# Optimization experiments

Hardware: AMD Instinct MI355X
Metric: run time of the kernel (lower is better)

## Reference

```python
import jax, jax.numpy as jnp
import numpy as np

B, N, M, K = 2, 16384, 16384, 32
C_IN, C_OUT, KS = 64, 128, 15
RADIUS = 0.1
SIGMA = 0.5 * RADIUS  # module sets self.sigma = sigma * radius


def _generate_kernel_points(num_kpoints: int, radius: float) -> np.ndarray:
    # Fibonacci-sphere placement, matching the torch generate_kernel_points
    if num_kpoints == 1:
        return np.zeros((1, 3), dtype=np.float32)
    pts = np.zeros((num_kpoints, 3), dtype=np.float32)
    golden_angle = np.pi * (3 - np.sqrt(5))
    for i in range(num_kpoints):
        y = 1 - i / float(num_kpoints - 1) * 2
        r_y = np.sqrt(1 - y * y)
        theta = golden_angle * i
        pts[i] = np.array([np.cos(theta) * r_y, y, np.sin(theta) * r_y]) * radius
    return pts


def setup_inputs() -> dict:
    key = jax.random.key(0)
    k1, k2, k3, k4 = jax.random.split(key, 4)
    query_points = jax.random.uniform(k1, (B, N, 3), dtype=jnp.float32)
    support_points = jax.random.uniform(k2, (B, M, 3), dtype=jnp.float32)
    support_features = jax.random.normal(k3, (B, M, C_IN), dtype=jnp.float32)
    neighbor_idx = jax.random.randint(k4, (B, N, K), 0, M)
    kernel_points = jnp.asarray(_generate_kernel_points(KS, RADIUS * 0.8))
    k5 = jax.random.fold_in(key, 5)
    # kaiming-uniform-ish init on flattened (KS*C_IN, C_OUT)
    bound = np.sqrt(1.0 / (KS * C_IN))
    weights = jax.random.uniform(k5, (KS, C_IN, C_OUT), dtype=jnp.float32,
                                 minval=-bound, maxval=bound)
    bias = jnp.zeros((C_OUT,), dtype=jnp.float32)
    return {
        "query_points": query_points,
        "support_points": support_points,
        "support_features": support_features,
        "neighbor_idx": neighbor_idx,
        "kernel_points": kernel_points,
        "weights": weights,
        "bias": bias,
    }


def reference(query_points, support_points, support_features, neighbor_idx,
              kernel_points, weights, bias):
    # Batched gather: support[b, idx[b]] -> [B, N, K, *]
    gather = jax.vmap(lambda feats, idx: feats[idx])
    neighbor_points = gather(support_points, neighbor_idx)      # [B,N,K,3]
    neighbor_features = gather(support_features, neighbor_idx)  # [B,N,K,C_in]

    rel = neighbor_points - query_points[:, :, None, :]          # [B,N,K,3]
    # squared distance to each kernel point: [B,N,K,J]
    sq_dist = jnp.sum((rel[:, :, :, None, :] - kernel_points[None, None, None]) ** 2,
                      axis=-1)
    influences = jnp.exp(-sq_dist / (2 * SIGMA ** 2))
    influences = influences / (influences.sum(axis=-1, keepdims=True) + 1e-6)

    out = jnp.einsum('bnkc,bnkj,jco->bno', neighbor_features, influences, weights)
    return out + bias
```

## Files before the change

### kernel.cpp

```cpp
#include <hip/hip_runtime.h>
#include <hip/hip_bf16.h>


#define NB   16384
#define MB   16384
#define KN   32
#define CIN  64
#define COUT 128
#define KS   15
#define TP   16
#define WF_BYTES  245760u
#define FP_BYTES  (2u * MB * CIN * 2u)
#define SP4_BYTES (2u * MB * 16u)

typedef __attribute__((ext_vector_type(8))) short short8;
typedef __attribute__((ext_vector_type(4))) float f32x4;

#define ROR_ADD(s, ctrl) \
    ((s) + __int_as_float(__builtin_amdgcn_update_dpp( \
        0, __float_as_int(s), (ctrl), 0xF, 0xF, true)))

static __device__ __forceinline__ unsigned int pack2_bf16(float f0, float f1) {
    const unsigned int a = __float_as_uint(f0) + 0x8000u;
    const unsigned int b = __float_as_uint(f1) + 0x8000u;
    return (a >> 16) | (b & 0xffff0000u);
}

static __device__ __forceinline__ unsigned int pack2_bf16_rne(float f0, float f1) {
    unsigned int a = __float_as_uint(f0);
    unsigned int b = __float_as_uint(f1);
    a += 0x7fffu + ((a >> 16) & 1u);
    b += 0x7fffu + ((b >> 16) & 1u);
    return (a >> 16) | (b & 0xffff0000u);
}

static __device__ __forceinline__ unsigned short f32_to_bf16_rne(float x) {
    unsigned int u = __float_as_uint(x);
    u += 0x7fffu + ((u >> 16) & 1u);
    return (unsigned short)(u >> 16);
}

__global__ __launch_bounds__(256)
void prep_kernel(const float* __restrict__ Wg, const float* __restrict__ feats,
                 const float* __restrict__ sp,
                 unsigned short* __restrict__ wf, unsigned int* __restrict__ fp,
                 float4* __restrict__ sp4, int full) {
    const int bid = blockIdx.x;
    if (bid < 60) {
        const int tid = bid * 256 + threadIdx.x;
        const int l = tid & 63;
        const int t = (tid >> 6) & 7;
        const int s = tid >> 9;
        const int n  = t * 16 + (l & 15);
        const int kb = s * 32 + (l >> 4) * 8;
        short8 o;
        #pragma unroll
        for (int i = 0; i < 8; ++i)
            o[i] = (short)f32_to_bf16_rne(Wg[(kb + i) * COUT + n]);
        *(short8*)(wf + (size_t)tid * 8) = o;
    } else if (!full) {
        return;
    } else if (bid < 60 + 128) {
        const int m = (bid - 60) * 256 + threadIdx.x;
        const float* s3 = sp + 3 * (size_t)m;
        sp4[m] = make_float4(s3[0], s3[1], s3[2], 0.0f);
    } else {
        const unsigned int t = (unsigned int)(bid - 188) * 256u + threadIdx.x;
        if (t < 2u * MB * 32u) {
            const int m   = t >> 5;
            const int p2  = t & 31;
            const int n16 = p2 >> 1;
            const int tt  = (p2 & 1) * 2;
            const float a = feats[(size_t)m * CIN + tt * 16 + n16];
            const float b = feats[(size_t)m * CIN + (tt + 1) * 16 + n16];
            fp[t] = pack2_bf16_rne(a, b);
        }
    }
}

template<bool PK>
__global__ __launch_bounds__(512, 6)
void kpconv_mfma(const float* __restrict__ qp,
                 const float* __restrict__ sp,
                 const float* __restrict__ feats,
                 const unsigned int* __restrict__ fpk,
                 const float4* __restrict__ sp4,
                 const int* __restrict__ nidx,
                 const float* __restrict__ kp,
                 const unsigned short* __restrict__ wfrag,
                 const float* __restrict__ bias,
                 float* __restrict__ out) {
    __shared__ __align__(16) char sF[16 * 2048];

    const int tid  = threadIdx.x;
    const int lane = tid & 63;
    const int wv   = tid >> 6;
    const int gp_base = blockIdx.x * TP;
    const int b = gp_base >> 14;
    const float*        fbf  = feats + (size_t)b * MB * CIN;
    const unsigned int* fpb  = fpk + (size_t)b * MB * 32;
    const float4*       sp4b = sp4 + (size_t)b * MB;
    const float*        spb  = sp + (size_t)b * MB * 3;

    const int n16  = lane & 15;
    const int quad = lane >> 4;

    float kxj, kyj, kzj;
    if (n16 < 15) {
        kxj = kp[3 * n16 + 0];
        kyj = kp[3 * n16 + 1];
        kzj = kp[3 * n16 + 2];
    } else {
        kxj = 1.0e4f; kyj = 1.0e4f; kzj = 1.0e4f;
    }

    const int gp0 = gp_base + wv * 2;
    const int* ip = nidx + (size_t)gp0 * KN + quad * 8;

    int idx0[8], idx1[8];
    *(int4*)(&idx0[0]) = *(const int4*)(ip);
    *(int4*)(&idx0[4]) = *(const int4*)(ip + 4);
    *(int4*)(&idx1[0]) = *(const int4*)(ip + KN);
    *(int4*)(&idx1[4]) = *(const int4*)(ip + KN + 4);

    #pragma unroll
    for (int pt = 0; pt < 2; ++pt) {
        const int pl = wv * 2 + pt;
        const int gp = gp0 + pt;
        const int* idxv = pt ? idx1 : idx0;

        const float qx = qp[3 * gp + 0];
        const float qy = qp[3 * gp + 1];
        const float qz = qp[3 * gp + 2];
        const float qkx = qx + kxj, qky = qy + kyj, qkz = qz + kzj;

        float e[8];
        uint2 g[8];
        if (PK) {
            float4 s4[8];
            #pragma unroll
            for (int i = 0; i < 8; ++i) s4[i] = sp4b[idxv[i]];
            #pragma unroll
            for (int i = 0; i < 8; ++i)
                g[i] = *(const uint2*)(fpb + (size_t)idxv[i] * 32 + n16 * 2);
            #pragma unroll
            for (int i = 0; i < 8; ++i) {
                const float dx = s4[i].x - qkx;
                const float dy = s4[i].y - qky;
                const float dz = s4[i].z - qkz;
                const float d2 = fmaf(dx, dx, fmaf(dy, dy, dz * dz));
                e[i] = __expf(-200.0f * d2);
            }
        } else {
            #pragma unroll
            for (int i = 0; i < 8; ++i) {
                const float* s3 = spb + (size_t)idxv[i] * 3;
                const float dx = s3[0] - qkx;
                const float dy = s3[1] - qky;
                const float dz = s3[2] - qkz;
                const float d2 = fmaf(dx, dx, fmaf(dy, dy, dz * dz));
                e[i] = __expf(-200.0f * d2);
            }
        }

        unsigned int iu[4];
        float en[8];
        #pragma unroll
        for (int i = 0; i < 8; ++i) {
            float s = e[i];
            s = ROR_ADD(s, 0x128);
            s = ROR_ADD(s, 0x124);
            s = ROR_ADD(s, 0x122);
            s = ROR_ADD(s, 0x121);
            en[i] = e[i] * __builtin_amdgcn_rcpf(s + 1e-6f);
        }
        #pragma unroll
        for (int ih = 0; ih < 4; ++ih)
            iu[ih] = pack2_bf16(en[2 * ih], en[2 * ih + 1]);
        const short8 ifrag = *(const short8*)iu;

        unsigned int fu[4][4];
        if (PK) {
            #pragma unroll
            for (int ih = 0; ih < 4; ++ih) {
                const unsigned int ax = g[2 * ih].x, bx = g[2 * ih + 1].x;
                const unsigned int ay = g[2 * ih].y, by = g[2 * ih + 1].y;
                fu[0][ih] = __builtin_amdgcn_perm(bx, ax, 0x05040100u);
                fu[1][ih] = __builtin_amdgcn_perm(bx, ax, 0x07060302u);
                fu[2][ih] = __builtin_amdgcn_perm(by, ay, 0x05040100u);
                fu[3][ih] = __builtin_amdgcn_perm(by, ay, 0x07060302u);
            }
        } else {
            #pragma unroll
            for (int ih = 0; ih < 4; ++ih) {
                const float* fr0 = fbf + (size_t)idxv[2 * ih]     * CIN + n16;
                const float* fr1 = fbf + (size_t)idxv[2 * ih + 1] * CIN + n16;
                #pragma unroll
                for (int t = 0; t < 4; ++t)
                    fu[t][ih] = pack2_bf16(fr0[t * 16], fr1[t * 16]);
            }
        }

        #pragma unroll
        for (int t = 0; t < 4; ++t) {
            const short8 ffrag = *(const short8*)(fu[t]);
            f32x4 z = {0.f, 0.f, 0.f, 0.f};
            const f32x4 dd = __builtin_amdgcn_mfma_f32_16x16x32_bf16(ffrag, ifrag, z, 0, 0, 0);
            const unsigned int lo = pack2_bf16(dd[0], dd[1]);
            const unsigned int hi = pack2_bf16(dd[2], dd[3]);
            const int off = n16 * 2048 + (t * 2 + (quad >> 1)) * 256 +
                            ((pl ^ (n16 & 7)) * 16) + (quad & 1) * 8;
            uint2 v; v.x = lo; v.y = hi;
            *(uint2*)(sF + off) = v;
        }
    }
    __syncthreads();

    f32x4 acc = {0.f, 0.f, 0.f, 0.f};

    #pragma unroll
    for (int s = 0; s < 30; ++s) {
        const int j = s >> 1;
        const int u = (s & 1) * 4 + quad;
        const int off = j * 2048 + u * 256 + ((n16 ^ (j & 7)) * 16);
        const short8 a  = *(const short8*)(sF + off);
        const short8 bf = *(const short8*)(wfrag + ((size_t)(s * 8 + wv) * 64 + lane) * 8);
        acc = __builtin_amdgcn_mfma_f32_16x16x32_bf16(a, bf, acc, 0, 0, 0);
    }

    const float bsv = bias[wv * 16 + n16];
    #pragma unroll
    for (int r = 0; r < 4; ++r) {
        out[(size_t)(gp_base + quad * 4 + r) * COUT + wv * 16 + n16] = acc[r] + bsv;
    }
}

extern "C" void kernel_launch(void* const* d_in, const int* in_sizes, int n_in,
                              void* d_out, int out_size, void* d_ws, size_t ws_size,
                              hipStream_t stream) {
    const float* qp = (const float*)d_in[0];
    const float* sp = (const float*)d_in[1];
    const float* ft = (const float*)d_in[2];
    const int*   ni = (const int*)d_in[3];
    const float* kp = (const float*)d_in[4];
    const float* wg = (const float*)d_in[5];
    const float* bs = (const float*)d_in[6];
    float* o = (float*)d_out;

    unsigned short* wfrag = (unsigned short*)d_ws;
    unsigned int*   fpk   = (unsigned int*)((char*)d_ws + WF_BYTES);
    float4*         sp4   = (float4*)((char*)d_ws + WF_BYTES + FP_BYTES);
    const int full = (ws_size >= (size_t)(WF_BYTES + FP_BYTES + SP4_BYTES)) ? 1 : 0;

    const int prep_blocks = full ? (60 + 128 + 4096) : 60;
    hipLaunchKernelGGL(prep_kernel, dim3(prep_blocks), dim3(256), 0, stream,
                       wg, ft, sp, wfrag, fpk, sp4, full);

    if (full) {
        hipLaunchKernelGGL((kpconv_mfma<true>), dim3((2 * NB) / TP), dim3(512), 0, stream,
                           qp, sp, ft, fpk, sp4, ni, kp, wfrag, bs, o);
    } else {
        hipLaunchKernelGGL((kpconv_mfma<false>), dim3((2 * NB) / TP), dim3(512), 0, stream,
                           qp, sp, ft, fpk, sp4, ni, kp, wfrag, bs, o);
    }
}
```

Baseline: 115.7 us.

## Process 32 points per block and software-pipeline neighbor gathers

Doubles the number of query points per block from 16 to 32, so each wave handles four points and the second-stage GEMM reuses each weight fragment load for two MFMAs. This halves weight-fragment traffic per point. It also software-pipelines the gather, prefetching the next point's neighbor indices and support-point coordinates while the current point is computed. In exchange it doubles LDS use, lowers the launch-bounds occupancy target from 6 to 4, and raises register pressure.

```diff
diff --git a/kernel.cpp b/kernel.cpp
--- a/kernel.cpp
+++ b/kernel.cpp
@@ -8,7 +8,7 @@
 #define CIN  64
 #define COUT 128
 #define KS   15
-#define TP   16
+#define TP   32
 #define WF_BYTES  245760u
 #define FP_BYTES  (2u * MB * CIN * 2u)
 #define SP4_BYTES (2u * MB * 16u)
@@ -79,7 +79,7 @@
 }
 
 template<bool PK>
-__global__ __launch_bounds__(512, 6)
+__global__ __launch_bounds__(512, 4)
 void kpconv_mfma(const float* __restrict__ qp,
                  const float* __restrict__ sp,
                  const float* __restrict__ feats,
@@ -90,7 +90,7 @@
                  const unsigned short* __restrict__ wfrag,
                  const float* __restrict__ bias,
                  float* __restrict__ out) {
-    __shared__ __align__(16) char sF[16 * 2048];
+    __shared__ __align__(16) char sF[16 * 4096];
 
     const int tid  = threadIdx.x;
     const int lane = tid & 63;
@@ -114,20 +114,44 @@
         kxj = 1.0e4f; kyj = 1.0e4f; kzj = 1.0e4f;
     }
 
-    const int gp0 = gp_base + wv * 2;
+    const int gp0 = gp_base + wv * 4;
     const int* ip = nidx + (size_t)gp0 * KN + quad * 8;
 
-    int idx0[8], idx1[8];
-    *(int4*)(&idx0[0]) = *(const int4*)(ip);
-    *(int4*)(&idx0[4]) = *(const int4*)(ip + 4);
-    *(int4*)(&idx1[0]) = *(const int4*)(ip + KN);
-    *(int4*)(&idx1[4]) = *(const int4*)(ip + KN + 4);
+    int idxc[8], idxn[8];
+    *(int4*)(&idxc[0]) = *(const int4*)(ip);
+    *(int4*)(&idxc[4]) = *(const int4*)(ip + 4);
+
+    float4 s4c[8];
+    if (PK) {
+        #pragma unroll
+        for (int i = 0; i < 8; ++i) s4c[i] = sp4b[idxc[i]];
+    }
+    *(int4*)(&idxn[0]) = *(const int4*)(ip + KN);
+    *(int4*)(&idxn[4]) = *(const int4*)(ip + KN + 4);
 
     #pragma unroll
-    for (int pt = 0; pt < 2; ++pt) {
-        const int pl = wv * 2 + pt;
+    for (int pt = 0; pt < 4; ++pt) {
+        const int pl = wv * 4 + pt;
         const int gp = gp0 + pt;
-        const int* idxv = pt ? idx1 : idx0;
+
+        uint2 g[8];
+        if (PK) {
+            #pragma unroll
+            for (int i = 0; i < 8; ++i)
+                g[i] = *(const uint2*)(fpb + (size_t)idxc[i] * 32 + n16 * 2);
+        }
+
+        float4 s4n[8];
+        if (PK && pt < 3) {
+            #pragma unroll
+            for (int i = 0; i < 8; ++i) s4n[i] = sp4b[idxn[i]];
+        }
+        int idx2[8];
+        if (pt < 2) {
+            const int* ip2 = ip + (pt + 2) * KN;
+            *(int4*)(&idx2[0]) = *(const int4*)(ip2);
+            *(int4*)(&idx2[4]) = *(const int4*)(ip2 + 4);
+        }
 
         const float qx = qp[3 * gp + 0];
         const float qy = qp[3 * gp + 1];
@@ -135,26 +159,19 @@
         const float qkx = qx + kxj, qky = qy + kyj, qkz = qz + kzj;
 
         float e[8];
-        uint2 g[8];
         if (PK) {
-            float4 s4[8];
-            #pragma unroll
-            for (int i = 0; i < 8; ++i) s4[i] = sp4b[idxv[i]];
-            #pragma unroll
-            for (int i = 0; i < 8; ++i)
-                g[i] = *(const uint2*)(fpb + (size_t)idxv[i] * 32 + n16 * 2);
             #pragma unroll
             for (int i = 0; i < 8; ++i) {
-                const float dx = s4[i].x - qkx;
-                const float dy = s4[i].y - qky;
-                const float dz = s4[i].z - qkz;
+                const float dx = s4c[i].x - qkx;
+                const float dy = s4c[i].y - qky;
+                const float dz = s4c[i].z - qkz;
                 const float d2 = fmaf(dx, dx, fmaf(dy, dy, dz * dz));
                 e[i] = __expf(-200.0f * d2);
             }
         } else {
             #pragma unroll
             for (int i = 0; i < 8; ++i) {
-                const float* s3 = spb + (size_t)idxv[i] * 3;
+                const float* s3 = spb + (size_t)idxc[i] * 3;
                 const float dx = s3[0] - qkx;
                 const float dy = s3[1] - qky;
                 const float dz = s3[2] - qkz;
@@ -193,8 +210,8 @@
         } else {
             #pragma unroll
             for (int ih = 0; ih < 4; ++ih) {
-                const float* fr0 = fbf + (size_t)idxv[2 * ih]     * CIN + n16;
-                const float* fr1 = fbf + (size_t)idxv[2 * ih + 1] * CIN + n16;
+                const float* fr0 = fbf + (size_t)idxc[2 * ih]     * CIN + n16;
+                const float* fr1 = fbf + (size_t)idxc[2 * ih + 1] * CIN + n16;
                 #pragma unroll
                 for (int t = 0; t < 4; ++t)
                     fu[t][ih] = pack2_bf16(fr0[t * 16], fr1[t * 16]);
@@ -208,30 +225,47 @@
             const f32x4 dd = __builtin_amdgcn_mfma_f32_16x16x32_bf16(ffrag, ifrag, z, 0, 0, 0);
             const unsigned int lo = pack2_bf16(dd[0], dd[1]);
             const unsigned int hi = pack2_bf16(dd[2], dd[3]);
-            const int off = n16 * 2048 + (t * 2 + (quad >> 1)) * 256 +
+            const int off = n16 * 4096 + (t * 2 + (quad >> 1)) * 512 +
                             ((pl ^ (n16 & 7)) * 16) + (quad & 1) * 8;
             uint2 v; v.x = lo; v.y = hi;
             *(uint2*)(sF + off) = v;
         }
+
+        if (pt < 3) {
+            #pragma unroll
+            for (int i = 0; i < 8; ++i) {
+                if (PK) s4c[i] = s4n[i];
+                idxc[i] = idxn[i];
+            }
+            if (pt < 2) {
+                #pragma unroll
+                for (int i = 0; i < 8; ++i) idxn[i] = idx2[i];
+            }
+        }
     }
     __syncthreads();
 
-    f32x4 acc = {0.f, 0.f, 0.f, 0.f};
+    f32x4 acc0 = {0.f, 0.f, 0.f, 0.f};
+    f32x4 acc1 = {0.f, 0.f, 0.f, 0.f};
 
     #pragma unroll
     for (int s = 0; s < 30; ++s) {
         const int j = s >> 1;
         const int u = (s & 1) * 4 + quad;
-        const int off = j * 2048 + u * 256 + ((n16 ^ (j & 7)) * 16);
-        const short8 a  = *(const short8*)(sF + off);
+        const int off0 = j * 4096 + u * 512 + ((n16 ^ (j & 7)) * 16);
+        const short8 a0 = *(const short8*)(sF + off0);
+        const short8 a1 = *(const short8*)(sF + off0 + 256);
         const short8 bf = *(const short8*)(wfrag + ((size_t)(s * 8 + wv) * 64 + lane) * 8);
-        acc = __builtin_amdgcn_mfma_f32_16x16x32_bf16(a, bf, acc, 0, 0, 0);
+        acc0 = __builtin_amdgcn_mfma_f32_16x16x32_bf16(a0, bf, acc0, 0, 0, 0);
+        acc1 = __builtin_amdgcn_mfma_f32_16x16x32_bf16(a1, bf, acc1, 0, 0, 0);
     }
 
     const float bsv = bias[wv * 16 + n16];
     #pragma unroll
     for (int r = 0; r < 4; ++r) {
-        out[(size_t)(gp_base + quad * 4 + r) * COUT + wv * 16 + n16] = acc[r] + bsv;
+        const int pr = quad * 4 + r;
+        out[(size_t)(gp_base + pr)      * COUT + wv * 16 + n16] = acc0[r] + bsv;
+        out[(size_t)(gp_base + 16 + pr) * COUT + wv * 16 + n16] = acc1[r] + bsv;
     }
 }
 
```

New measurement: 109.2 us. 5.7% less time.

## Process two 16-point halves per block with double-buffered LDS software pipeline

Applied to the files above, without the earlier changes.

Each block now handles 32 query points in two halves, each with its own LDS buffer. The index and support-point gathers for the second half are issued before the first half's weight MFMA stage, so global gather latency overlaps with matrix work. The cost is double the LDS footprint (64KB), a lower occupancy hint, and half as many blocks. The launch configuration must also change to match the new block size.

```diff
diff --git a/kernel.cpp b/kernel.cpp
--- a/kernel.cpp
+++ b/kernel.cpp
@@ -8,7 +8,7 @@
 #define CIN  64
 #define COUT 128
 #define KS   15
-#define TP   16
+#define TP   32
 #define WF_BYTES  245760u
 #define FP_BYTES  (2u * MB * CIN * 2u)
 #define SP4_BYTES (2u * MB * 16u)
@@ -79,7 +79,7 @@
 }
 
 template<bool PK>
-__global__ __launch_bounds__(512, 6)
+__global__ __launch_bounds__(512, 4)
 void kpconv_mfma(const float* __restrict__ qp,
                  const float* __restrict__ sp,
                  const float* __restrict__ feats,
@@ -90,7 +90,7 @@
                  const unsigned short* __restrict__ wfrag,
                  const float* __restrict__ bias,
                  float* __restrict__ out) {
-    __shared__ __align__(16) char sF[16 * 2048];
+    __shared__ __align__(16) char sF[2 * 32768];
 
     const int tid  = threadIdx.x;
     const int lane = tid & 63;
@@ -113,21 +113,40 @@
     } else {
         kxj = 1.0e4f; kyj = 1.0e4f; kzj = 1.0e4f;
     }
-
-    const int gp0 = gp_base + wv * 2;
-    const int* ip = nidx + (size_t)gp0 * KN + quad * 8;
-
-    int idx0[8], idx1[8];
-    *(int4*)(&idx0[0]) = *(const int4*)(ip);
-    *(int4*)(&idx0[4]) = *(const int4*)(ip + 4);
-    *(int4*)(&idx1[0]) = *(const int4*)(ip + KN);
-    *(int4*)(&idx1[4]) = *(const int4*)(ip + KN + 4);
-
-    #pragma unroll
-    for (int pt = 0; pt < 2; ++pt) {
-        const int pl = wv * 2 + pt;
-        const int gp = gp0 + pt;
-        const int* idxv = pt ? idx1 : idx0;
+    const float bsv = bias[wv * 16 + n16];
+
+    int idxA[8], idxB[8];
+    float4 s4A[8];
+
+    auto loadPair = [&](int h) {
+        const int gp = gp_base + h * 16 + wv * 2;
+        const int* ipp = nidx + (size_t)gp * KN + quad * 8;
+        *(int4*)(&idxA[0]) = *(const int4*)(ipp);
+        *(int4*)(&idxA[4]) = *(const int4*)(ipp + 4);
+        *(int4*)(&idxB[0]) = *(const int4*)(ipp + KN);
+        *(int4*)(&idxB[4]) = *(const int4*)(ipp + KN + 4);
+    };
+
+    auto gatherSp4 = [&](const int* idxv, float4* s4) {
+        if (PK) {
+            #pragma unroll
+            for (int i = 0; i < 8; ++i) s4[i] = sp4b[idxv[i]];
+        } else {
+            #pragma unroll
+            for (int i = 0; i < 8; ++i) {
+                const float* s3 = spb + (size_t)idxv[i] * 3;
+                s4[i] = make_float4(s3[0], s3[1], s3[2], 0.0f);
+            }
+        }
+    };
+
+    auto aPoint = [&](const int* idxv, const float4* s4, int h, int plh, int gp) {
+        uint2 g[8];
+        if (PK) {
+            #pragma unroll
+            for (int i = 0; i < 8; ++i)
+                g[i] = *(const uint2*)(fpb + (size_t)idxv[i] * 32 + n16 * 2);
+        }
 
         const float qx = qp[3 * gp + 0];
         const float qy = qp[3 * gp + 1];
@@ -135,32 +154,13 @@
         const float qkx = qx + kxj, qky = qy + kyj, qkz = qz + kzj;
 
         float e[8];
-        uint2 g[8];
-        if (PK) {
-            float4 s4[8];
-            #pragma unroll
-            for (int i = 0; i < 8; ++i) s4[i] = sp4b[idxv[i]];
-            #pragma unroll
-            for (int i = 0; i < 8; ++i)
-                g[i] = *(const uint2*)(fpb + (size_t)idxv[i] * 32 + n16 * 2);
-            #pragma unroll
-            for (int i = 0; i < 8; ++i) {
-                const float dx = s4[i].x - qkx;
-                const float dy = s4[i].y - qky;
-                const float dz = s4[i].z - qkz;
-                const float d2 = fmaf(dx, dx, fmaf(dy, dy, dz * dz));
-                e[i] = __expf(-200.0f * d2);
-            }
-        } else {
-            #pragma unroll
-            for (int i = 0; i < 8; ++i) {
-                const float* s3 = spb + (size_t)idxv[i] * 3;
-                const float dx = s3[0] - qkx;
-                const float dy = s3[1] - qky;
-                const float dz = s3[2] - qkz;
-                const float d2 = fmaf(dx, dx, fmaf(dy, dy, dz * dz));
-                e[i] = __expf(-200.0f * d2);
-            }
+        #pragma unroll
+        for (int i = 0; i < 8; ++i) {
+            const float dx = s4[i].x - qkx;
+            const float dy = s4[i].y - qky;
+            const float dz = s4[i].z - qkz;
+            const float d2 = fmaf(dx, dx, fmaf(dy, dy, dz * dz));
+            e[i] = __expf(-200.0f * d2);
         }
 
         unsigned int iu[4];
@@ -201,6 +201,7 @@
             }
         }
 
+        char* base = sF + h * 32768;
         #pragma unroll
         for (int t = 0; t < 4; ++t) {
             const short8 ffrag = *(const short8*)(fu[t]);
@@ -209,30 +210,50 @@
             const unsigned int lo = pack2_bf16(dd[0], dd[1]);
             const unsigned int hi = pack2_bf16(dd[2], dd[3]);
             const int off = n16 * 2048 + (t * 2 + (quad >> 1)) * 256 +
-                            ((pl ^ (n16 & 7)) * 16) + (quad & 1) * 8;
+                            ((plh ^ (n16 & 7)) * 16) + (quad & 1) * 8;
             uint2 v; v.x = lo; v.y = hi;
-            *(uint2*)(sF + off) = v;
-        }
-    }
+            *(uint2*)(base + off) = v;
+        }
+    };
+
+    auto aHalf = [&](int h) {
+        float4 s4B[8];
+        gatherSp4(idxB, s4B);
+        aPoint(idxA, s4A, h, wv * 2,     gp_base + h * 16 + wv * 2);
+        aPoint(idxB, s4B, h, wv * 2 + 1, gp_base + h * 16 + wv * 2 + 1);
+    };
+
+    auto bHalf = [&](int h) {
+        f32x4 acc = {0.f, 0.f, 0.f, 0.f};
+        const char* base = sF + h * 32768;
+        #pragma unroll
+        for (int s = 0; s < 30; ++s) {
+            const int j = s >> 1;
+            const int u = (s & 1) * 4 + quad;
+            const short8 a  = *(const short8*)(base + j * 2048 + u * 256 +
+                                               ((n16 ^ (j & 7)) * 16));
+            const short8 bf = *(const short8*)(wfrag +
+                                ((size_t)(s * 8 + wv) * 64 + lane) * 8);
+            acc = __builtin_amdgcn_mfma_f32_16x16x32_bf16(a, bf, acc, 0, 0, 0);
+        }
+        #pragma unroll
+        for (int r = 0; r < 4; ++r)
+            out[(size_t)(gp_base + h * 16 + quad * 4 + r) * COUT + wv * 16 + n16]
+                = acc[r] + bsv;
+    };
+
+    loadPair(0);
+    gatherSp4(idxA, s4A);
+    aHalf(0);
     __syncthreads();
 
-    f32x4 acc = {0.f, 0.f, 0.f, 0.f};
-
-    #pragma unroll
-    for (int s = 0; s < 30; ++s) {
-        const int j = s >> 1;
-        const int u = (s & 1) * 4 + quad;
-        const int off = j * 2048 + u * 256 + ((n16 ^ (j & 7)) * 16);
-        const short8 a  = *(const short8*)(sF + off);
-        const short8 bf = *(const short8*)(wfrag + ((size_t)(s * 8 + wv) * 64 + lane) * 8);
-        acc = __builtin_amdgcn_mfma_f32_16x16x32_bf16(a, bf, acc, 0, 0, 0);
-    }
-
-    const float bsv = bias[wv * 16 + n16];
-    #pragma unroll
-    for (int r = 0; r < 4; ++r) {
-        out[(size_t)(gp_base + quad * 4 + r) * COUT + wv * 16 + n16] = acc[r] + bsv;
-    }
+    loadPair(1);
+    gatherSp4(idxA, s4A);
+    bHalf(0);
+    aHalf(1);
+    __syncthreads();
+
+    bHalf(1);
 }
 
 extern "C" void kernel_launch(void* const* d_in, const int* in_sizes, int n_in,
```

Result: slower. 131.6 us (+13.7%).

## Process two point tiles per block with double-buffered LDS to overlap gathers

Applied to the files above, without the earlier changes.

Each block now handles 32 query points in two halves of 16, using two LDS buffers. The index loads and support-point gathers for the second half are issued before the first half's weight GEMM, so gather latency can overlap MFMA work. Occupancy drops from 6 to 4 blocks per CU in launch bounds and LDS use doubles. The interpolation code is also restructured to interleave pairs of DPP reductions for more instruction-level parallelism.

```diff
diff --git a/kernel.cpp b/kernel.cpp
--- a/kernel.cpp
+++ b/kernel.cpp
@@ -8,7 +8,7 @@
 #define CIN  64
 #define COUT 128
 #define KS   15
-#define TP   16
+#define TP   32
 #define WF_BYTES  245760u
 #define FP_BYTES  (2u * MB * CIN * 2u)
 #define SP4_BYTES (2u * MB * 16u)
@@ -78,8 +78,121 @@
     }
 }
 
+
+#define LOAD_IDX_PAIR(IDX0, IDX1, GPH)                                        \
+    {                                                                         \
+        const int* ipp_ = nidx + (size_t)(GPH) * KN + quad * 8;               \
+        *(int4*)(&IDX0[0]) = *(const int4*)(ipp_);                            \
+        *(int4*)(&IDX0[4]) = *(const int4*)(ipp_ + 4);                        \
+        *(int4*)(&IDX1[0]) = *(const int4*)(ipp_ + KN);                       \
+        *(int4*)(&IDX1[4]) = *(const int4*)(ipp_ + KN + 4);                   \
+    }
+
+#define GATHER_SP4(IDXV, S4V)                                                 \
+    {                                                                         \
+        if (PK) {                                                             \
+            _Pragma("unroll")                                                 \
+            for (int i_ = 0; i_ < 8; ++i_) S4V[i_] = sp4b[IDXV[i_]];          \
+        } else {                                                              \
+            _Pragma("unroll")                                                 \
+            for (int i_ = 0; i_ < 8; ++i_) {                                  \
+                const float* s3_ = spb + (size_t)IDXV[i_] * 3;                \
+                S4V[i_] = make_float4(s3_[0], s3_[1], s3_[2], 0.0f);          \
+            }                                                                 \
+        }                                                                     \
+    }
+
+#define A_POINT(IDXV, S4V, BASE, PLH, GP)                                     \
+    {                                                                         \
+        uint2 g_[8];                                                          \
+        if (PK) {                                                             \
+            _Pragma("unroll")                                                 \
+            for (int i_ = 0; i_ < 8; ++i_)                                    \
+                g_[i_] = *(const uint2*)(fpb + (size_t)IDXV[i_] * 32 + n16 * 2); \
+        }                                                                     \
+        const float qx_ = qp[3 * (GP) + 0];                                   \
+        const float qy_ = qp[3 * (GP) + 1];                                   \
+        const float qz_ = qp[3 * (GP) + 2];                                   \
+        const float qkx_ = qx_ + kxj, qky_ = qy_ + kyj, qkz_ = qz_ + kzj;     \
+        float e_[8];                                                          \
+        _Pragma("unroll")                                                     \
+        for (int i_ = 0; i_ < 8; ++i_) {                                      \
+            const float dx_ = S4V[i_].x - qkx_;                               \
+            const float dy_ = S4V[i_].y - qky_;                               \
+            const float dz_ = S4V[i_].z - qkz_;                               \
+            const float d2_ = fmaf(dx_, dx_, fmaf(dy_, dy_, dz_ * dz_));      \
+            e_[i_] = __expf(-200.0f * d2_);                                   \
+        }                                                                     \
+        unsigned int iu_[4];                                                  \
+        _Pragma("unroll")                                                     \
+        for (int ih_ = 0; ih_ < 4; ++ih_) {                                   \
+            float s0_ = e_[2 * ih_], s1_ = e_[2 * ih_ + 1];                   \
+            s0_ = ROR_ADD(s0_, 0x128); s1_ = ROR_ADD(s1_, 0x128);             \
+            s0_ = ROR_ADD(s0_, 0x124); s1_ = ROR_ADD(s1_, 0x124);             \
+            s0_ = ROR_ADD(s0_, 0x122); s1_ = ROR_ADD(s1_, 0x122);             \
+            s0_ = ROR_ADD(s0_, 0x121); s1_ = ROR_ADD(s1_, 0x121);             \
+            const float n0_ = e_[2 * ih_]     * __builtin_amdgcn_rcpf(s0_ + 1e-6f); \
+            const float n1_ = e_[2 * ih_ + 1] * __builtin_amdgcn_rcpf(s1_ + 1e-6f); \
+            iu_[ih_] = pack2_bf16(n0_, n1_);                                  \
+        }                                                                     \
+        const short8 ifrag_ = *(const short8*)iu_;                            \
+        unsigned int fu_[4][4];                                               \
+        if (PK) {                                                             \
+            _Pragma("unroll")                                                 \
+            for (int ih_ = 0; ih_ < 4; ++ih_) {                               \
+                const unsigned int ax_ = g_[2 * ih_].x, bx_ = g_[2 * ih_ + 1].x; \
+                const unsigned int ay_ = g_[2 * ih_].y, by_ = g_[2 * ih_ + 1].y; \
+                fu_[0][ih_] = __builtin_amdgcn_perm(bx_, ax_, 0x05040100u);   \
+                fu_[1][ih_] = __builtin_amdgcn_perm(bx_, ax_, 0x07060302u);   \
+                fu_[2][ih_] = __builtin_amdgcn_perm(by_, ay_, 0x05040100u);   \
+                fu_[3][ih_] = __builtin_amdgcn_perm(by_, ay_, 0x07060302u);   \
+            }                                                                 \
+        } else {                                                              \
+            _Pragma("unroll")                                                 \
+            for (int ih_ = 0; ih_ < 4; ++ih_) {                               \
+                const float* fr0_ = fbf + (size_t)IDXV[2 * ih_]     * CIN + n16; \
+                const float* fr1_ = fbf + (size_t)IDXV[2 * ih_ + 1] * CIN + n16; \
+                _Pragma("unroll")                                             \
+                for (int t_ = 0; t_ < 4; ++t_)                                \
+                    fu_[t_][ih_] = pack2_bf16(fr0_[t_ * 16], fr1_[t_ * 16]);  \
+            }                                                                 \
+        }                                                                     \
+        _Pragma("unroll")                                                     \
+        for (int t_ = 0; t_ < 4; ++t_) {                                      \
+            const short8 ffrag_ = *(const short8*)(fu_[t_]);                  \
+            f32x4 z_ = {0.f, 0.f, 0.f, 0.f};                                  \
+            const f32x4 dd_ = __builtin_amdgcn_mfma_f32_16x16x32_bf16(        \
+                ffrag_, ifrag_, z_, 0, 0, 0);                                 \
+            const unsigned int lo_ = pack2_bf16(dd_[0], dd_[1]);              \
+            const unsigned int hi_ = pack2_bf16(dd_[2], dd_[3]);              \
+            const int off_ = n16 * 2048 + (t_ * 2 + (quad >> 1)) * 256 +      \
+                             (((PLH) ^ (n16 & 7)) * 16) + (quad & 1) * 8;     \
+            uint2 v_; v_.x = lo_; v_.y = hi_;                                 \
+            *(uint2*)((BASE) + off_) = v_;                                    \
+        }                                                                     \
+    }
+
+#define B_HALF(BASE, ROW0)                                                    \
+    {                                                                         \
+        f32x4 acc_ = {0.f, 0.f, 0.f, 0.f};                                    \
+        _Pragma("unroll")                                                     \
+        for (int s_ = 0; s_ < 30; ++s_) {                                     \
+            const int j_ = s_ >> 1;                                           \
+            const int u_ = (s_ & 1) * 4 + quad;                               \
+            const short8 a_ = *(const short8*)((BASE) + j_ * 2048 + u_ * 256 +\
+                                               ((n16 ^ (j_ & 7)) * 16));      \
+            const short8 bf_ = *(const short8*)(wfrag +                       \
+                                ((size_t)(s_ * 8 + wv) * 64 + lane) * 8);     \
+            acc_ = __builtin_amdgcn_mfma_f32_16x16x32_bf16(a_, bf_, acc_, 0, 0, 0); \
+        }                                                                     \
+        _Pragma("unroll")                                                     \
+        for (int r_ = 0; r_ < 4; ++r_)                                        \
+            out[(size_t)((ROW0) + quad * 4 + r_) * COUT + wv * 16 + n16]      \
+                = acc_[r_] + bsv;                                             \
+    }
+
 template<bool PK>
-__global__ __launch_bounds__(512, 6)
+__global__ __launch_bounds__(512, 4)
 void kpconv_mfma(const float* __restrict__ qp,
                  const float* __restrict__ sp,
                  const float* __restrict__ feats,
@@ -90,7 +203,7 @@
                  const unsigned short* __restrict__ wfrag,
                  const float* __restrict__ bias,
                  float* __restrict__ out) {
-    __shared__ __align__(16) char sF[16 * 2048];
+    __shared__ __align__(16) char sF[2 * 32768];
 
     const int tid  = threadIdx.x;
     const int lane = tid & 63;
@@ -113,126 +226,32 @@
     } else {
         kxj = 1.0e4f; kyj = 1.0e4f; kzj = 1.0e4f;
     }
-
-    const int gp0 = gp_base + wv * 2;
-    const int* ip = nidx + (size_t)gp0 * KN + quad * 8;
-
-    int idx0[8], idx1[8];
-    *(int4*)(&idx0[0]) = *(const int4*)(ip);
-    *(int4*)(&idx0[4]) = *(const int4*)(ip + 4);
-    *(int4*)(&idx1[0]) = *(const int4*)(ip + KN);
-    *(int4*)(&idx1[4]) = *(const int4*)(ip + KN + 4);
-
-    #pragma unroll
-    for (int pt = 0; pt < 2; ++pt) {
-        const int pl = wv * 2 + pt;
-        const int gp = gp0 + pt;
-        const int* idxv = pt ? idx1 : idx0;
-
-        const float qx = qp[3 * gp + 0];
-        const float qy = qp[3 * gp + 1];
-        const float qz = qp[3 * gp + 2];
-        const float qkx = qx + kxj, qky = qy + kyj, qkz = qz + kzj;
-
-        float e[8];
-        uint2 g[8];
-        if (PK) {
-            float4 s4[8];
-            #pragma unroll
-            for (int i = 0; i < 8; ++i) s4[i] = sp4b[idxv[i]];
-            #pragma unroll
-            for (int i = 0; i < 8; ++i)
-                g[i] = *(const uint2*)(fpb + (size_t)idxv[i] * 32 + n16 * 2);
-            #pragma unroll
-            for (int i = 0; i < 8; ++i) {
-                const float dx = s4[i].x - qkx;
-                const float dy = s4[i].y - qky;
-                const float dz = s4[i].z - qkz;
-                const float d2 = fmaf(dx, dx, fmaf(dy, dy, dz * dz));
-                e[i] = __expf(-200.0f * d2);
-            }
-        } else {
-            #pragma unroll
-            for (int i = 0; i < 8; ++i) {
-                const float* s3 = spb + (size_t)idxv[i] * 3;
-                const float dx = s3[0] - qkx;
-                const float dy = s3[1] - qky;
-                const float dz = s3[2] - qkz;
-                const float d2 = fmaf(dx, dx, fmaf(dy, dy, dz * dz));
-                e[i] = __expf(-200.0f * d2);
-            }
-        }
-
-        unsigned int iu[4];
-        float en[8];
-        #pragma unroll
-        for (int i = 0; i < 8; ++i) {
-            float s = e[i];
-            s = ROR_ADD(s, 0x128);
-            s = ROR_ADD(s, 0x124);
-            s = ROR_ADD(s, 0x122);
-            s = ROR_ADD(s, 0x121);
-            en[i] = e[i] * __builtin_amdgcn_rcpf(s + 1e-6f);
-        }
-        #pragma unroll
-        for (int ih = 0; ih < 4; ++ih)
-            iu[ih] = pack2_bf16(en[2 * ih], en[2 * ih + 1]);
-        const short8 ifrag = *(const short8*)iu;
-
-        unsigned int fu[4][4];
-        if (PK) {
-            #pragma unroll
-            for (int ih = 0; ih < 4; ++ih) {
-                const unsigned int ax = g[2 * ih].x, bx = g[2 * ih + 1].x;
-                const unsigned int ay = g[2 * ih].y, by = g[2 * ih + 1].y;
-                fu[0][ih] = __builtin_amdgcn_perm(bx, ax, 0x05040100u);
-                fu[1][ih] = __builtin_amdgcn_perm(bx, ax, 0x07060302u);
-                fu[2][ih] = __builtin_amdgcn_perm(by, ay, 0x05040100u);
-                fu[3][ih] = __builtin_amdgcn_perm(by, ay, 0x07060302u);
-            }
-        } else {
-            #pragma unroll
-            for (int ih = 0; ih < 4; ++ih) {
-                const float* fr0 = fbf + (size_t)idxv[2 * ih]     * CIN + n16;
-                const float* fr1 = fbf + (size_t)idxv[2 * ih + 1] * CIN + n16;
-                #pragma unroll
-                for (int t = 0; t < 4; ++t)
-                    fu[t][ih] = pack2_bf16(fr0[t * 16], fr1[t * 16]);
-            }
-        }
-
-        #pragma unroll
-        for (int t = 0; t < 4; ++t) {
-            const short8 ffrag = *(const short8*)(fu[t]);
-            f32x4 z = {0.f, 0.f, 0.f, 0.f};
-            const f32x4 dd = __builtin_amdgcn_mfma_f32_16x16x32_bf16(ffrag, ifrag, z, 0, 0, 0);
-            const unsigned int lo = pack2_bf16(dd[0], dd[1]);
-            const unsigned int hi = pack2_bf16(dd[2], dd[3]);
-            const int off = n16 * 2048 + (t * 2 + (quad >> 1)) * 256 +
-                            ((pl ^ (n16 & 7)) * 16) + (quad & 1) * 8;
-            uint2 v; v.x = lo; v.y = hi;
-            *(uint2*)(sF + off) = v;
-        }
-    }
+    const float bsv = bias[wv * 16 + n16];
+
+    int idxA0[8], idxB0[8];
+    float4 s4A0[8], s4B0[8];
+    const int gph0 = gp_base + wv * 2;
+    LOAD_IDX_PAIR(idxA0, idxB0, gph0);
+    GATHER_SP4(idxA0, s4A0);
+    GATHER_SP4(idxB0, s4B0);
+    A_POINT(idxA0, s4A0, sF, wv * 2,     gph0);
+    A_POINT(idxB0, s4B0, sF, wv * 2 + 1, gph0 + 1);
     __syncthreads();
 
-    f32x4 acc = {0.f, 0.f, 0.f, 0.f};
-
-    #pragma unroll
-    for (int s = 0; s < 30; ++s) {
-        const int j = s >> 1;
-        const int u = (s & 1) * 4 + quad;
-        const int off = j * 2048 + u * 256 + ((n16 ^ (j & 7)) * 16);
-        const short8 a  = *(const short8*)(sF + off);
-        const short8 bf = *(const short8*)(wfrag + ((size_t)(s * 8 + wv) * 64 + lane) * 8);
-        acc = __builtin_amdgcn_mfma_f32_16x16x32_bf16(a, bf, acc, 0, 0, 0);
-    }
-
-    const float bsv = bias[wv * 16 + n16];
-    #pragma unroll
-    for (int r = 0; r < 4; ++r) {
-        out[(size_t)(gp_base + quad * 4 + r) * COUT + wv * 16 + n16] = acc[r] + bsv;
-    }
+    int idxA1[8], idxB1[8];
+    float4 s4A1[8], s4B1[8];
+    const int gph1 = gp_base + 16 + wv * 2;
+    LOAD_IDX_PAIR(idxA1, idxB1, gph1);
+    GATHER_SP4(idxA1, s4A1);
+    GATHER_SP4(idxB1, s4B1);
+
+    B_HALF(sF, gp_base);
+
+    A_POINT(idxA1, s4A1, sF + 32768, wv * 2,     gph1);
+    A_POINT(idxB1, s4B1, sF + 32768, wv * 2 + 1, gph1 + 1);
+    __syncthreads();
+
+    B_HALF(sF + 32768, gp_base + 16);
 }
 
 extern "C" void kernel_launch(void* const* d_in, const int* in_sizes, int n_in,
```

Result: slower. 131.3 us (+13.4%).
